# Optimization experiments

Measured on AMD Instinct MI355X. Metric: run time of the kernel, lower is better.

Reference implementation:

```python
import jax, jax.numpy as jnp
import numpy as np

B, T, C = 128, 384, 256
H, KV, D = 4, 2, 64          # n_head, n_kv_head, head_dim
REP = H // KV                # query heads per kv head
BLOCK_SIZE = 384


def setup_inputs() -> dict:
    key = jax.random.key(0)
    k0, k1, k2, k3, k4 = jax.random.split(key, 5)
    scale = 0.02
    return {
        "x":  jax.random.normal(k0, (B, T, C), jnp.float32),
        "Wq": jax.random.normal(k1, (C, H * D), jnp.float32) * scale,
        "Wk": jax.random.normal(k2, (C, KV * D), jnp.float32) * scale,
        "Wv": jax.random.normal(k3, (C, KV * D), jnp.float32) * scale,
        "Wo": jax.random.normal(k4, (C, C), jnp.float32) * scale,
    }


def _rope_tables(t_len):
    inv_freq = 1.0 / (10000.0 ** (jnp.arange(0, D, 2, dtype=jnp.float32) / D))
    t = jnp.arange(t_len, dtype=jnp.float32)
    freqs = jnp.outer(t, inv_freq)            # [T, D/2]
    emb = jnp.concatenate([freqs, freqs], -1)  # [T, D]
    return jnp.cos(emb), jnp.sin(emb)


def _rotate_half(x):
    h = x.shape[-1] // 2
    return jnp.concatenate([-x[..., h:], x[..., :h]], -1)


def _apply_rope(x, cos, sin):
    # x: [B, heads, T, D]; cos/sin: [T, D]
    return x * cos[None, None] + _rotate_half(x) * sin[None, None]


def reference(x, Wq, Wk, Wv, Wo):
    b, t, c = x.shape
    q = (x @ Wq).reshape(b, t, H, D).transpose(0, 2, 1, 3)   # [B,H,T,D]
    k = (x @ Wk).reshape(b, t, KV, D).transpose(0, 2, 1, 3)  # [B,KV,T,D]
    v = (x @ Wv).reshape(b, t, KV, D).transpose(0, 2, 1, 3)

    cos, sin = _rope_tables(t)
    q = _apply_rope(q, cos, sin)
    k = _apply_rope(k, cos, sin)

    # GQA: group query heads by kv head instead of repeat_interleave on K/V.
    qg = q.reshape(b, KV, REP, t, D)
    scores = jnp.einsum('bgrtd,bgsd->bgrts', qg, k) / jnp.sqrt(jnp.float32(D))
    causal = jnp.tril(jnp.ones((t, t), dtype=bool))
    scores = jnp.where(causal, scores, jnp.finfo(scores.dtype).min)
    p = jax.nn.softmax(scores, axis=-1)
    y = jnp.einsum('bgrts,bgsd->bgrtd', p, v)                 # [B,KV,REP,T,D]
    y = y.reshape(b, H, t, D).transpose(0, 2, 1, 3).reshape(b, t, c)
    return y @ Wo
```

## Files before the change

kernel.cpp:

```cpp
#include <hip/hip_runtime.h>
#include <hip/hip_bf16.h>

#define BB 128
#define TT 384
#define CC 256
#define HH 4
#define KVH 2
#define QKVW 512
#define MROWS (BB * TT)

#define CVT_BLOCKS 6144

typedef __attribute__((ext_vector_type(8))) short short8;
typedef __attribute__((ext_vector_type(4))) float float4v;

__device__ __forceinline__ unsigned short f2b(float f) {
    union { float f; unsigned u; } v; v.f = f;
    unsigned u = v.u;
    unsigned r = (u + 0x7fffu + ((u >> 16) & 1u)) >> 16;
    return (unsigned short)r;
}
__device__ __forceinline__ float b2f(unsigned short s) {
    union { unsigned u; float f; } v; v.u = ((unsigned)s) << 16;
    return v.f;
}
__device__ __forceinline__ float4v mfma16(short8 a, short8 b, float4v c) {
    return __builtin_amdgcn_mfma_f32_16x16x32_bf16(a, b, c, 0, 0, 0);
}
__device__ __forceinline__ void g2lds16(const void* g, void* l) {
    __builtin_amdgcn_global_load_lds(
        (const __attribute__((address_space(1))) unsigned int*)g,
        (__attribute__((address_space(3))) unsigned int*)l, 16, 0, 0);
}

__global__ void prep_kernel(const float* __restrict__ x, unsigned short* __restrict__ xb,
                            const float* __restrict__ Wq, const float* __restrict__ Wk,
                            const float* __restrict__ Wv, const float* __restrict__ Wo,
                            unsigned short* __restrict__ WqkvT, unsigned short* __restrict__ WoT,
                            float* __restrict__ cosT, float* __restrict__ sinT) {
    if (blockIdx.x < CVT_BLOCKS) {
        size_t e = ((size_t)blockIdx.x * 256 + threadIdx.x) * 8;
        const float4* p = (const float4*)(x + e);
        float4 v0 = p[0], v1 = p[1];
        short8 w;
        w[0]=(short)f2b(v0.x); w[1]=(short)f2b(v0.y); w[2]=(short)f2b(v0.z); w[3]=(short)f2b(v0.w);
        w[4]=(short)f2b(v1.x); w[5]=(short)f2b(v1.y); w[6]=(short)f2b(v1.z); w[7]=(short)f2b(v1.w);
        *(short8*)(xb + e) = w;
        return;
    }
    int idx = (blockIdx.x - CVT_BLOCKS) * 256 + threadIdx.x;
    const int N1 = QKVW * CC;
    const int N2 = N1 + CC * CC;
    const int N3 = N2 + TT * 32;
    if (idx < N1) {
        int n = idx >> 8, k = idx & 255;
        float w;
        if (n < 256)      w = Wq[k * 256 + n];
        else if (n < 384) w = Wk[k * 128 + (n - 256)];
        else              w = Wv[k * 128 + (n - 384)];
        WqkvT[n * 256 + k] = f2b(w);
    } else if (idx < N2) {
        int i = idx - N1; int n = i >> 8, k = i & 255;
        WoT[n * 256 + k] = f2b(Wo[k * 256 + n]);
    } else if (idx < N3) {
        int i = idx - N2;
        int t = i >> 5, f = i & 31;
        double invf = exp2(-(double)f / 32.0 * 13.287712379549449);
        double ang = (double)t * invf;
        cosT[t * 32 + f] = (float)cos(ang);
        sinT[t * 32 + f] = (float)sin(ang);
    }
}

__global__ __launch_bounds__(256) void gemm_qkv_kernel(
    const unsigned short* __restrict__ A, const unsigned short* __restrict__ BT,
    unsigned short* __restrict__ Qr, unsigned short* __restrict__ Kr,
    unsigned short* __restrict__ Vt,
    const float* __restrict__ cosT, const float* __restrict__ sinT)
{
    __shared__ __align__(16) unsigned short As[128 * 32];
    __shared__ __align__(16) unsigned short Bs[128 * 32];
    const int tid  = threadIdx.x;
    const int lane = tid & 63;
    const int quad = lane >> 4, l16 = lane & 15;
    const int wave = tid >> 6;
    const int mt = blockIdx.x >> 2, nt = blockIdx.x & 3;
    const int mbase = mt * 128, nbase = nt * 128;
    const int wmb = (wave >> 1) * 64, wnb = (wave & 1) * 64;

    float4v acc[4][4] = {};
    const int r0 = tid >> 2, kc = (tid & 3) * 8;
    const int ldsW = (tid & ~63) * 16;
    const unsigned short* gA0 = A  + (size_t)(mbase + r0) * CC + kc;
    const unsigned short* gB0 = BT + (size_t)(nbase + r0) * CC + kc;

    for (int kt = 0; kt < CC; kt += 32) {
        __syncthreads();
        g2lds16(gA0 + kt,                  (char*)As + ldsW);
        g2lds16(gA0 + kt + (size_t)64*CC,  (char*)As + 4096 + ldsW);
        g2lds16(gB0 + kt,                  (char*)Bs + ldsW);
        g2lds16(gB0 + kt + (size_t)64*CC,  (char*)Bs + 4096 + ldsW);
        __syncthreads();

        short8 af[4], bf_[4];
        #pragma unroll
        for (int i = 0; i < 4; i++)
            af[i] = *(const short8*)&As[(wmb + i * 16 + l16) * 32 + quad * 8];
        #pragma unroll
        for (int i = 0; i < 4; i++)
            bf_[i] = *(const short8*)&Bs[(wnb + i * 16 + l16) * 32 + quad * 8];
        #pragma unroll
        for (int i = 0; i < 4; i++)
            #pragma unroll
            for (int j = 0; j < 4; j++)
                acc[i][j] = mfma16(af[i], bf_[j], acc[i][j]);
    }

    const int gn0 = nbase + wnb;
    const int gm0 = mbase + wmb;
    if (gn0 < 384) {
        const bool isq = (gn0 < 256);
        const int  hh  = isq ? (gn0 >> 6) : ((gn0 - 256) >> 6);
        const float qs = isq ? 0.18033688011112042f : 1.0f;
        #pragma unroll
        for (int i = 0; i < 4; i++) {
            #pragma unroll
            for (int r = 0; r < 4; r++) {
                int gm = gm0 + i * 16 + quad * 4 + r;
                int b = gm / TT, t = gm - b * TT;
                unsigned short* dst = isq
                    ? (Qr + (((size_t)b * HH  + hh) * TT + t) * 64)
                    : (Kr + (((size_t)b * KVH + hh) * TT + t) * 64);
                #pragma unroll
                for (int j = 0; j < 2; j++) {
                    int f = j * 16 + l16;
                    float cs = cosT[t * 32 + f], sn = sinT[t * 32 + f];
                    float a  = acc[i][j][r],     c2 = acc[i][j + 2][r];
                    dst[f]      = f2b((a * cs - c2 * sn) * qs);
                    dst[f + 32] = f2b((c2 * cs + a * sn) * qs);
                }
            }
        }
    } else {
        const int g = (gn0 - 384) >> 6;
        #pragma unroll
        for (int i = 0; i < 4; i++) {
            #pragma unroll
            for (int r = 0; r < 4; r++) {
                int gm = gm0 + i * 16 + quad * 4 + r;
                int b = gm / TT, s = gm - b * TT;
                unsigned short* dst = Vt + (((size_t)b * KVH + g) * 6 + (s >> 6)) * 4096 + (s & 63);
                #pragma unroll
                for (int j = 0; j < 4; j++)
                    dst[(j * 16 + l16) * 64] = f2b(acc[i][j][r]);
            }
        }
    }
}

__global__ __launch_bounds__(256) void gemm_out_kernel(
    const unsigned short* __restrict__ A, const unsigned short* __restrict__ BT,
    float* __restrict__ C)
{
    __shared__ __align__(16) unsigned short As[128 * 32];
    __shared__ __align__(16) unsigned short Bs[128 * 32];
    const int tid  = threadIdx.x;
    const int lane = tid & 63;
    const int quad = lane >> 4, l16 = lane & 15;
    const int wave = tid >> 6;
    const int mt = blockIdx.x >> 1, nt = blockIdx.x & 1;
    const int mbase = mt * 128, nbase = nt * 128;
    const int wmb = (wave >> 1) * 64, wnb = (wave & 1) * 64;

    float4v acc[4][4] = {};
    const int r0 = tid >> 2, kc = (tid & 3) * 8;
    const int ldsW = (tid & ~63) * 16;
    const unsigned short* gA0 = A  + (size_t)(mbase + r0) * CC + kc;
    const unsigned short* gB0 = BT + (size_t)(nbase + r0) * CC + kc;

    for (int kt = 0; kt < CC; kt += 32) {
        __syncthreads();
        g2lds16(gA0 + kt,                  (char*)As + ldsW);
        g2lds16(gA0 + kt + (size_t)64*CC,  (char*)As + 4096 + ldsW);
        g2lds16(gB0 + kt,                  (char*)Bs + ldsW);
        g2lds16(gB0 + kt + (size_t)64*CC,  (char*)Bs + 4096 + ldsW);
        __syncthreads();

        short8 af[4], bf_[4];
        #pragma unroll
        for (int i = 0; i < 4; i++)
            af[i] = *(const short8*)&As[(wmb + i * 16 + l16) * 32 + quad * 8];
        #pragma unroll
        for (int i = 0; i < 4; i++)
            bf_[i] = *(const short8*)&Bs[(wnb + i * 16 + l16) * 32 + quad * 8];
        #pragma unroll
        for (int i = 0; i < 4; i++)
            #pragma unroll
            for (int j = 0; j < 4; j++)
                acc[i][j] = mfma16(af[i], bf_[j], acc[i][j]);
    }
    #pragma unroll
    for (int i = 0; i < 4; i++)
        #pragma unroll
        for (int j = 0; j < 4; j++)
            #pragma unroll
            for (int r = 0; r < 4; r++)
                C[(size_t)(mbase + wmb + i * 16 + quad * 4 + r) * CC + nbase + wnb + j * 16 + l16]
                    = acc[i][j][r];
}

__global__ __launch_bounds__(256) void attn_kernel(
    const unsigned short* __restrict__ Qr, const unsigned short* __restrict__ Kr,
    const unsigned short* __restrict__ Vt, unsigned short* __restrict__ y)
{
    __shared__ __align__(16) unsigned short Ks[64 * 64];
    __shared__ __align__(16) unsigned short Vs[64 * 64];
    __shared__ __align__(16) unsigned short Ps[4][32 * 64];

    const int tid  = threadIdx.x;
    const int lane = tid & 63;
    const int wave = tid >> 6;
    const int quad = lane >> 4, l16 = lane & 15;

    const int bid = blockIdx.x;
    const int qt = bid % 6;
    const int g  = (bid / 6) & 1;
    const int b  = bid / 12;
    const int h  = g * 2 + (wave >> 1);
    const int qbase = qt * 64 + (wave & 1) * 32;

    short8 qf[2][2];
    #pragma unroll
    for (int mi = 0; mi < 2; mi++)
        #pragma unroll
        for (int half = 0; half < 2; half++)
            qf[mi][half] = *(const short8*)(Qr
                + (((size_t)b * HH + h) * TT + qbase + mi * 16 + l16) * 64 + half * 32 + quad * 8);

    float4v acc[2][4] = {};
    float4v accl[2]   = {};
    short8 ones;
    #pragma unroll
    for (int j = 0; j < 8; j++) ones[j] = (short)0x3F80;

    const unsigned short* Kbase = Kr + ((size_t)b * KVH + g) * TT * 64;
    const unsigned short* Vbase = Vt + ((size_t)b * KVH + g) * 6 * 4096;
    char* Pw = (char*)&Ps[wave][0];
    const int ldsWave = (tid & ~63) * 16;

    for (int kt = 0; kt <= qt; kt++) {
        __syncthreads();
        #pragma unroll
        for (int it = 0; it < 2; it++) {
            int L  = it * 256 + tid;
            int gc = (L & ~7) | ((L & 7) ^ ((L >> 3) & 7));
            g2lds16(Kbase + (size_t)kt * 4096 + gc * 8, (char*)Ks + it * 4096 + ldsWave);
            g2lds16(Vbase + (size_t)kt * 4096 + gc * 8, (char*)Vs + it * 4096 + ldsWave);
        }
        __syncthreads();

        float4v s_[2][4];
        #pragma unroll
        for (int js = 0; js < 4; js++) {
            int srow = js * 16 + l16, sw = srow & 7;
            short8 kb0 = *(const short8*)((char*)Ks + srow * 128 + ((quad ^ sw) * 16));
            short8 kb1 = *(const short8*)((char*)Ks + srow * 128 + (((4 + quad) ^ sw) * 16));
            #pragma unroll
            for (int mi = 0; mi < 2; mi++) {
                float4v z = {};
                z = mfma16(qf[mi][0], kb0, z);
                s_[mi][js] = mfma16(qf[mi][1], kb1, z);
            }
        }

        if (kt == qt) {
            #pragma unroll
            for (int mi = 0; mi < 2; mi++)
                #pragma unroll
                for (int js = 0; js < 4; js++) {
                    int coll = js * 16 + l16;
                    #pragma unroll
                    for (int r = 0; r < 4; r++) {
                        int rowl = (wave & 1) * 32 + mi * 16 + quad * 4 + r;
                        if (coll > rowl) s_[mi][js][r] = -1e30f;
                    }
                }
        }

        #pragma unroll
        for (int mi = 0; mi < 2; mi++)
            #pragma unroll
            for (int js = 0; js < 4; js++)
                #pragma unroll
                for (int r = 0; r < 4; r++) {
                    float p = exp2f(s_[mi][js][r]);
                    int prow = mi * 16 + quad * 4 + r;
                    int c8 = (js * 2 + (l16 >> 3)) ^ (prow & 7);
                    *(unsigned short*)(Pw + prow * 128 + c8 * 16 + (l16 & 7) * 2) = f2b(p);
                }

        short8 pa[2][2];
        #pragma unroll
        for (int mi = 0; mi < 2; mi++)
            #pragma unroll
            for (int half = 0; half < 2; half++) {
                int prow = mi * 16 + l16;
                int c8 = ((half * 4 + quad) ^ (prow & 7));
                pa[mi][half] = *(const short8*)(Pw + prow * 128 + c8 * 16);
            }
        #pragma unroll
        for (int dj = 0; dj < 4; dj++) {
            int vrow = dj * 16 + l16, sw = vrow & 7;
            short8 vb0 = *(const short8*)((char*)Vs + vrow * 128 + ((quad ^ sw) * 16));
            short8 vb1 = *(const short8*)((char*)Vs + vrow * 128 + (((4 + quad) ^ sw) * 16));
            #pragma unroll
            for (int mi = 0; mi < 2; mi++) {
                acc[mi][dj] = mfma16(pa[mi][0], vb0, acc[mi][dj]);
                acc[mi][dj] = mfma16(pa[mi][1], vb1, acc[mi][dj]);
            }
        }
        #pragma unroll
        for (int mi = 0; mi < 2; mi++) {
            accl[mi] = mfma16(pa[mi][0], ones, accl[mi]);
            accl[mi] = mfma16(pa[mi][1], ones, accl[mi]);
        }
    }

    #pragma unroll
    for (int mi = 0; mi < 2; mi++) {
        float rinv[4];
        #pragma unroll
        for (int r = 0; r < 4; r++) rinv[r] = 1.0f / accl[mi][r];
        #pragma unroll
        for (int dj = 0; dj < 4; dj++)
            #pragma unroll
            for (int r = 0; r < 4; r++) {
                int t = qbase + mi * 16 + quad * 4 + r;
                y[((size_t)b * TT + t) * CC + h * 64 + dj * 16 + l16]
                    = f2b(acc[mi][dj][r] * rinv[r]);
            }
    }
}

extern "C" void kernel_launch(void* const* d_in, const int* in_sizes, int n_in,
                              void* d_out, int out_size, void* d_ws, size_t ws_size,
                              hipStream_t stream) {
    const float* x  = (const float*)d_in[0];
    const float* Wq = (const float*)d_in[1];
    const float* Wk = (const float*)d_in[2];
    const float* Wv = (const float*)d_in[3];
    const float* Wo = (const float*)d_in[4];
    float* out = (float*)d_out;

    char* ws = (char*)d_ws;
    size_t off = 0;
    unsigned short* xb = (unsigned short*)(ws + off); off += (size_t)MROWS * CC * 2;
    unsigned short* Qr = (unsigned short*)(ws + off); off += (size_t)BB * HH  * TT * 64 * 2;
    unsigned short* Kr = (unsigned short*)(ws + off); off += (size_t)BB * KVH * TT * 64 * 2;
    unsigned short* Vt = (unsigned short*)(ws + off); off += (size_t)BB * KVH * TT * 64 * 2;
    unsigned short* y  = (unsigned short*)(ws + off); off += (size_t)MROWS * CC * 2;
    unsigned short* WqkvT = (unsigned short*)(ws + off); off += (size_t)QKVW * CC * 2;
    unsigned short* WoT   = (unsigned short*)(ws + off); off += (size_t)CC * CC * 2;
    float* cosT = (float*)(ws + off); off += (size_t)TT * 32 * 4;
    float* sinT = (float*)(ws + off); off += (size_t)TT * 32 * 4;

    prep_kernel<<<CVT_BLOCKS + 816, 256, 0, stream>>>(x, xb, Wq, Wk, Wv, Wo,
                                                      WqkvT, WoT, cosT, sinT);
    gemm_qkv_kernel<<<(MROWS / 128) * 4, 256, 0, stream>>>(xb, WqkvT, Qr, Kr, Vt, cosT, sinT);
    attn_kernel<<<BB * KVH * 6, 256, 0, stream>>>(Qr, Kr, Vt, y);
    gemm_out_kernel<<<(MROWS / 128) * 2, 256, 0, stream>>>(y, WoT, out);
}
```

Before: 186.4 us.

## Pair causal query tiles per block, double-buffer KV tiles, swizzle GEMM block order

The attention kernel now has each block handle two query tiles (qt=5-p and qt=p), so every block does the same amount of causal work. One K/V load feeds both tiles, which halves the grid and reduces redundant K/V traffic. K/V tiles are double-buffered in LDS so the next tile's global loads overlap the current compute, with one barrier per iteration. P is written as packed bf16 pairs via a perm-based conversion with a new swizzle, and the V layout in the QKV epilogue is permuted. Both GEMMs remap block indices into groups of 8 M-tiles for L2 locality. This adds register pressure (two accumulator sets) and raises LDS use, with launch_bounds set to 3 blocks per CU.

Result: slower. 194.5 us (+4.3%).

```diff
diff --git a/kernel.cpp b/kernel.cpp
--- a/kernel.cpp
+++ b/kernel.cpp
@@ -20,10 +20,6 @@
     unsigned r = (u + 0x7fffu + ((u >> 16) & 1u)) >> 16;
     return (unsigned short)r;
 }
-__device__ __forceinline__ float b2f(unsigned short s) {
-    union { unsigned u; float f; } v; v.u = ((unsigned)s) << 16;
-    return v.f;
-}
 __device__ __forceinline__ float4v mfma16(short8 a, short8 b, float4v c) {
     return __builtin_amdgcn_mfma_f32_16x16x32_bf16(a, b, c, 0, 0, 0);
 }
@@ -31,6 +27,10 @@
     __builtin_amdgcn_global_load_lds(
         (const __attribute__((address_space(1))) unsigned int*)g,
         (__attribute__((address_space(3))) unsigned int*)l, 16, 0, 0);
+}
+__device__ __forceinline__ unsigned pk2bf(float a, float b) {
+    union { float f; unsigned u; } x, y; x.f = a; y.f = b;
+    return __builtin_amdgcn_perm(y.u + 0x8000u, x.u + 0x8000u, 0x07060302u);
 }
 
 __global__ void prep_kernel(const float* __restrict__ x, unsigned short* __restrict__ xb,
@@ -84,7 +84,8 @@
     const int lane = tid & 63;
     const int quad = lane >> 4, l16 = lane & 15;
     const int wave = tid >> 6;
-    const int mt = blockIdx.x >> 2, nt = blockIdx.x & 3;
+    const int mt = ((blockIdx.x >> 5) << 3) | (blockIdx.x & 7);
+    const int nt = (blockIdx.x >> 3) & 3;
     const int mbase = mt * 128, nbase = nt * 128;
     const int wmb = (wave >> 1) * 64, wnb = (wave & 1) * 64;
 
@@ -149,7 +150,9 @@
             for (int r = 0; r < 4; r++) {
                 int gm = gm0 + i * 16 + quad * 4 + r;
                 int b = gm / TT, s = gm - b * TT;
-                unsigned short* dst = Vt + (((size_t)b * KVH + g) * 6 + (s >> 6)) * 4096 + (s & 63);
+                int s6 = s & 63;
+                int sig = (s6 & 15) * 4 + (s6 >> 4);
+                unsigned short* dst = Vt + (((size_t)b * KVH + g) * 6 + (s >> 6)) * 4096 + sig;
                 #pragma unroll
                 for (int j = 0; j < 4; j++)
                     dst[(j * 16 + l16) * 64] = f2b(acc[i][j][r]);
@@ -168,7 +171,8 @@
     const int lane = tid & 63;
     const int quad = lane >> 4, l16 = lane & 15;
     const int wave = tid >> 6;
-    const int mt = blockIdx.x >> 1, nt = blockIdx.x & 1;
+    const int mt = ((blockIdx.x >> 4) << 3) | (blockIdx.x & 7);
+    const int nt = (blockIdx.x >> 3) & 1;
     const int mbase = mt * 128, nbase = nt * 128;
     const int wmb = (wave >> 1) * 64, wnb = (wave & 1) * 64;
 
@@ -209,12 +213,12 @@
                     = acc[i][j][r];
 }
 
-__global__ __launch_bounds__(256) void attn_kernel(
+__global__ __launch_bounds__(256, 3) void attn_kernel(
     const unsigned short* __restrict__ Qr, const unsigned short* __restrict__ Kr,
     const unsigned short* __restrict__ Vt, unsigned short* __restrict__ y)
 {
-    __shared__ __align__(16) unsigned short Ks[64 * 64];
-    __shared__ __align__(16) unsigned short Vs[64 * 64];
+    __shared__ __align__(16) unsigned short Ks[2][64 * 64];
+    __shared__ __align__(16) unsigned short Vs[2][64 * 64];
     __shared__ __align__(16) unsigned short Ps[4][32 * 64];
 
     const int tid  = threadIdx.x;
@@ -222,23 +226,31 @@
     const int wave = tid >> 6;
     const int quad = lane >> 4, l16 = lane & 15;
 
-    const int bid = blockIdx.x;
-    const int qt = bid % 6;
-    const int g  = (bid / 6) & 1;
-    const int b  = bid / 12;
-    const int h  = g * 2 + (wave >> 1);
-    const int qbase = qt * 64 + (wave & 1) * 32;
-
-    short8 qf[2][2];
+    const int xc  = blockIdx.x & 7;
+    const int jj  = blockIdx.x >> 3;
+    const int p   = jj % 3;
+    const int bg  = (jj / 3) * 8 + xc;
+    const int g   = bg & 1, b = bg >> 1;
+    const int h   = g * 2 + (wave >> 1);
+    const int qtA = 5 - p, qtB = p;
+    const int qbA = qtA * 64 + (wave & 1) * 32;
+    const int qbB = qtB * 64 + (wave & 1) * 32;
+
+    short8 qf[2][2][2];
     #pragma unroll
-    for (int mi = 0; mi < 2; mi++)
-        #pragma unroll
-        for (int half = 0; half < 2; half++)
-            qf[mi][half] = *(const short8*)(Qr
-                + (((size_t)b * HH + h) * TT + qbase + mi * 16 + l16) * 64 + half * 32 + quad * 8);
-
-    float4v acc[2][4] = {};
-    float4v accl[2]   = {};
+    for (int t = 0; t < 2; t++) {
+        int qb = t ? qbB : qbA;
+        #pragma unroll
+        for (int mi = 0; mi < 2; mi++)
+            #pragma unroll
+            for (int half = 0; half < 2; half++)
+                qf[t][mi][half] = *(const short8*)(Qr
+                    + (((size_t)b * HH + h) * TT + qb + mi * 16 + l16) * 64
+                    + half * 32 + quad * 8);
+    }
+
+    float4v acc[2][2][4] = {};
+    float4v accl[2][2]   = {};
     short8 ones;
     #pragma unroll
     for (int j = 0; j < 8; j++) ones[j] = (short)0x3F80;
@@ -247,33 +259,35 @@
     const unsigned short* Vbase = Vt + ((size_t)b * KVH + g) * 6 * 4096;
     char* Pw = (char*)&Ps[wave][0];
     const int ldsWave = (tid & ~63) * 16;
-
-    for (int kt = 0; kt <= qt; kt++) {
-        __syncthreads();
-        #pragma unroll
-        for (int it = 0; it < 2; it++) {
-            int L  = it * 256 + tid;
-            int gc = (L & ~7) | ((L & 7) ^ ((L >> 3) & 7));
-            g2lds16(Kbase + (size_t)kt * 4096 + gc * 8, (char*)Ks + it * 4096 + ldsWave);
-            g2lds16(Vbase + (size_t)kt * 4096 + gc * 8, (char*)Vs + it * 4096 + ldsWave);
-        }
-        __syncthreads();
-
+    int gc0, gc1;
+    { int L0 = tid;       gc0 = ((L0 & ~7) | ((L0 & 7) ^ ((L0 >> 3) & 7))) * 8;
+      int L1 = 256 + tid; gc1 = ((L1 & ~7) | ((L1 & 7) ^ ((L1 >> 3) & 7))) * 8; }
+
+    auto stage = [&](int bi, int kt) {
+        const unsigned short* kB = Kbase + (size_t)kt * 4096;
+        const unsigned short* vB = Vbase + (size_t)kt * 4096;
+        g2lds16(kB + gc0, (char*)&Ks[bi][0] + ldsWave);
+        g2lds16(kB + gc1, (char*)&Ks[bi][0] + 4096 + ldsWave);
+        g2lds16(vB + gc0, (char*)&Vs[bi][0] + ldsWave);
+        g2lds16(vB + gc1, (char*)&Vs[bi][0] + 4096 + ldsWave);
+    };
+
+    auto computeTile = [&](int t, const unsigned short* Kc, const unsigned short* Vc,
+                           bool domask) {
         float4v s_[2][4];
         #pragma unroll
         for (int js = 0; js < 4; js++) {
             int srow = js * 16 + l16, sw = srow & 7;
-            short8 kb0 = *(const short8*)((char*)Ks + srow * 128 + ((quad ^ sw) * 16));
-            short8 kb1 = *(const short8*)((char*)Ks + srow * 128 + (((4 + quad) ^ sw) * 16));
+            short8 kb0 = *(const short8*)((const char*)Kc + srow * 128 + ((quad ^ sw) * 16));
+            short8 kb1 = *(const short8*)((const char*)Kc + srow * 128 + (((4 + quad) ^ sw) * 16));
             #pragma unroll
             for (int mi = 0; mi < 2; mi++) {
                 float4v z = {};
-                z = mfma16(qf[mi][0], kb0, z);
-                s_[mi][js] = mfma16(qf[mi][1], kb1, z);
-            }
-        }
-
-        if (kt == qt) {
+                z = mfma16(qf[t][mi][0], kb0, z);
+                s_[mi][js] = mfma16(qf[t][mi][1], kb1, z);
+            }
+        }
+        if (domask) {
             #pragma unroll
             for (int mi = 0; mi < 2; mi++)
                 #pragma unroll
@@ -286,59 +300,74 @@
                     }
                 }
         }
-
         #pragma unroll
         for (int mi = 0; mi < 2; mi++)
             #pragma unroll
-            for (int js = 0; js < 4; js++)
+            for (int r = 0; r < 4; r++) {
+                float e0 = __builtin_amdgcn_exp2f(s_[mi][0][r]);
+                float e1 = __builtin_amdgcn_exp2f(s_[mi][1][r]);
+                float e2 = __builtin_amdgcn_exp2f(s_[mi][2][r]);
+                float e3 = __builtin_amdgcn_exp2f(s_[mi][3][r]);
+                unsigned long long d =
+                    (unsigned long long)pk2bf(e0, e1) |
+                    ((unsigned long long)pk2bf(e2, e3) << 32);
+                int rho = mi * 16 + quad * 4 + r;
+                int ch  = l16 ^ (((quad * 4 + r) & 7) << 1);
+                *(unsigned long long*)(Pw + rho * 128 + ch * 8) = d;
+            }
+        short8 pa[2][2];
+        #pragma unroll
+        for (int mi = 0; mi < 2; mi++)
+            #pragma unroll
+            for (int half = 0; half < 2; half++) {
+                int chp = (2 * (half * 4 + quad)) ^ ((l16 & 7) << 1);
+                pa[mi][half] = *(const short8*)(Pw + (mi * 16 + l16) * 128 + chp * 8);
+            }
+        #pragma unroll
+        for (int dj = 0; dj < 4; dj++) {
+            int vrow = dj * 16 + l16, sw = vrow & 7;
+            short8 vb0 = *(const short8*)((const char*)Vc + vrow * 128 + ((quad ^ sw) * 16));
+            short8 vb1 = *(const short8*)((const char*)Vc + vrow * 128 + (((4 + quad) ^ sw) * 16));
+            #pragma unroll
+            for (int mi = 0; mi < 2; mi++) {
+                acc[t][mi][dj] = mfma16(pa[mi][0], vb0, acc[t][mi][dj]);
+                acc[t][mi][dj] = mfma16(pa[mi][1], vb1, acc[t][mi][dj]);
+            }
+        }
+        #pragma unroll
+        for (int mi = 0; mi < 2; mi++) {
+            accl[t][mi] = mfma16(pa[mi][0], ones, accl[t][mi]);
+            accl[t][mi] = mfma16(pa[mi][1], ones, accl[t][mi]);
+        }
+    };
+
+    stage(0, 0);
+    for (int kt = 0; kt <= qtA; kt++) {
+        __syncthreads();
+        if (kt < qtA) stage((kt + 1) & 1, kt + 1);
+        const unsigned short* Kc = &Ks[kt & 1][0];
+        const unsigned short* Vc = &Vs[kt & 1][0];
+        computeTile(0, Kc, Vc, kt == qtA);
+        if (kt <= qtB) computeTile(1, Kc, Vc, kt == qtB);
+    }
+
+    #pragma unroll
+    for (int t = 0; t < 2; t++) {
+        int qb = t ? qbB : qbA;
+        #pragma unroll
+        for (int mi = 0; mi < 2; mi++) {
+            float rinv[4];
+            #pragma unroll
+            for (int r = 0; r < 4; r++) rinv[r] = 1.0f / accl[t][mi][r];
+            #pragma unroll
+            for (int dj = 0; dj < 4; dj++)
                 #pragma unroll
                 for (int r = 0; r < 4; r++) {
-                    float p = exp2f(s_[mi][js][r]);
-                    int prow = mi * 16 + quad * 4 + r;
-                    int c8 = (js * 2 + (l16 >> 3)) ^ (prow & 7);
-                    *(unsigned short*)(Pw + prow * 128 + c8 * 16 + (l16 & 7) * 2) = f2b(p);
+                    int tt = qb + mi * 16 + quad * 4 + r;
+                    y[((size_t)b * TT + tt) * CC + h * 64 + dj * 16 + l16]
+                        = f2b(acc[t][mi][dj][r] * rinv[r]);
                 }
-
-        short8 pa[2][2];
-        #pragma unroll
-        for (int mi = 0; mi < 2; mi++)
-            #pragma unroll
-            for (int half = 0; half < 2; half++) {
-                int prow = mi * 16 + l16;
-                int c8 = ((half * 4 + quad) ^ (prow & 7));
-                pa[mi][half] = *(const short8*)(Pw + prow * 128 + c8 * 16);
-            }
-        #pragma unroll
-        for (int dj = 0; dj < 4; dj++) {
-            int vrow = dj * 16 + l16, sw = vrow & 7;
-            short8 vb0 = *(const short8*)((char*)Vs + vrow * 128 + ((quad ^ sw) * 16));
-            short8 vb1 = *(const short8*)((char*)Vs + vrow * 128 + (((4 + quad) ^ sw) * 16));
-            #pragma unroll
-            for (int mi = 0; mi < 2; mi++) {
-                acc[mi][dj] = mfma16(pa[mi][0], vb0, acc[mi][dj]);
-                acc[mi][dj] = mfma16(pa[mi][1], vb1, acc[mi][dj]);
-            }
-        }
-        #pragma unroll
-        for (int mi = 0; mi < 2; mi++) {
-            accl[mi] = mfma16(pa[mi][0], ones, accl[mi]);
-            accl[mi] = mfma16(pa[mi][1], ones, accl[mi]);
-        }
-    }
-
-    #pragma unroll
-    for (int mi = 0; mi < 2; mi++) {
-        float rinv[4];
-        #pragma unroll
-        for (int r = 0; r < 4; r++) rinv[r] = 1.0f / accl[mi][r];
-        #pragma unroll
-        for (int dj = 0; dj < 4; dj++)
-            #pragma unroll
-            for (int r = 0; r < 4; r++) {
-                int t = qbase + mi * 16 + quad * 4 + r;
-                y[((size_t)b * TT + t) * CC + h * 64 + dj * 16 + l16]
-                    = f2b(acc[mi][dj][r] * rinv[r]);
-            }
+        }
     }
 }
 
@@ -367,6 +396,6 @@
     prep_kernel<<<CVT_BLOCKS + 816, 256, 0, stream>>>(x, xb, Wq, Wk, Wv, Wo,
                                                       WqkvT, WoT, cosT, sinT);
     gemm_qkv_kernel<<<(MROWS / 128) * 4, 256, 0, stream>>>(xb, WqkvT, Qr, Kr, Vt, cosT, sinT);
-    attn_kernel<<<BB * KVH * 6, 256, 0, stream>>>(Qr, Kr, Vt, y);
+    attn_kernel<<<BB * KVH * 3, 256, 0, stream>>>(Qr, Kr, Vt, y);
     gemm_out_kernel<<<(MROWS / 128) * 2, 256, 0, stream>>>(y, WoT, out);
 }
```
